# Optimization experiments

Measured on AMD Instinct MI355X. Metric: run time of the kernel, lower is better.

## Reference

```python
import jax, jax.numpy as jnp
import numpy as np

B, N, E, T, DS, H = 32, 1024, 16384, 8, 8, 32
EPS = 1e-12

def setup_inputs() -> dict:
    key = jax.random.key(0)
    ks = jax.random.split(key, 10)
    xyz = jax.random.normal(ks[0], (B, N, 3), dtype=jnp.float32)
    edge_index = jax.random.randint(ks[1], (2, E), 0, N)
    edge_type = jax.random.randint(ks[2], (E,), 0, T)
    edge_rest_lengths = jax.random.uniform(ks[3], (E,), dtype=jnp.float32) + 0.5
    type_emb = 0.1 * jax.random.normal(ks[4], (T, DS), dtype=jnp.float32)
    w1 = 0.1 * jax.random.normal(ks[5], (3 + DS, H), dtype=jnp.float32)
    b1 = jnp.zeros((H,), dtype=jnp.float32)
    w2 = 0.1 * jax.random.normal(ks[6], (H,), dtype=jnp.float32)
    b2 = jnp.zeros((1,), dtype=jnp.float32)
    default_bias = 0.1 * jax.random.normal(ks[7], (1,), dtype=jnp.float32)
    return {"xyz": xyz, "edge_index": edge_index, "edge_type": edge_type,
            "edge_rest_lengths": edge_rest_lengths, "type_emb": type_emb,
            "w1": w1, "b1": b1, "w2": w2, "b2": b2, "default_bias": default_bias}

def reference(xyz, edge_index, edge_type, edge_rest_lengths, type_emb, w1, b1, w2, b2, default_bias):
    src, dst = edge_index[0], edge_index[1]           # (E,)
    diff = xyz[:, dst, :] - xyz[:, src, :]            # (B,E,3) edge gather
    dist = jnp.sqrt(jnp.sum(diff * diff, axis=-1) + EPS)  # (B,E)
    rest = jnp.broadcast_to(edge_rest_lengths, dist.shape)  # (B,E)
    geo = jnp.stack([dist, rest, dist - rest], axis=-1)     # (B,E,3)
    struct = jnp.broadcast_to(type_emb[edge_type], (dist.shape[0], E, type_emb.shape[1]))  # (B,E,DS)
    feats = jnp.concatenate([geo, struct], axis=-1)   # (B,E,3+DS)
    h = jax.nn.relu(jnp.einsum('bef,fh->beh', feats, w1) + b1)  # (B,E,H)
    score = jnp.einsum('beh,h->be', h, w2) + b2       # (B,E)
    # dense bias with learnable default fill, symmetric edge scatter
    bias = default_bias * jnp.ones((xyz.shape[0], N, N), dtype=xyz.dtype)
    bias = bias.at[:, src, dst].set(score)
    bias = bias.at[:, dst, src].set(score)
    return bias[:, None, :, :]                        # (B,1,N,N)
```

## Files before the change

kernel.cpp:

```cpp
#include <hip/hip_runtime.h>

#define BB 32
#define NN 1024
#define EE 16384
#define DSS 8
#define HH 32


__global__ void init_prio(int* __restrict__ prio) {
    int idx = blockIdx.x * blockDim.x + threadIdx.x;
    ((int4*)prio)[idx] = make_int4(-1, -1, -1, -1);
}

__global__ void build_prio(const int* __restrict__ edge_index, int* __restrict__ prio) {
    int t = blockIdx.x * blockDim.x + threadIdx.x;
    int pass = t >= EE;
    int e = t - pass * EE;
    int src = edge_index[e];
    int dst = edge_index[EE + e];
    int i = pass ? dst : src;
    int j = pass ? src : dst;
    atomicMax(&prio[i * NN + j], t);
}

__global__ void score_kernel(const float* __restrict__ xyz,
                             const int* __restrict__ edge_index,
                             const int* __restrict__ edge_type,
                             const float* __restrict__ rest_len,
                             const float* __restrict__ type_emb,
                             const float* __restrict__ w1,
                             const float* __restrict__ b1,
                             const float* __restrict__ w2,
                             const float* __restrict__ b2,
                             float* __restrict__ score) {
    int idx = blockIdx.x * blockDim.x + threadIdx.x;
    int e = idx & (EE - 1);
    int b = idx >> 14;
    int src = edge_index[e];
    int dst = edge_index[EE + e];
    const float* ps = xyz + ((size_t)b * NN + src) * 3;
    const float* pd = xyz + ((size_t)b * NN + dst) * 3;
    float dx = pd[0] - ps[0];
    float dy = pd[1] - ps[1];
    float dz = pd[2] - ps[2];
    float dist = sqrtf(dx * dx + dy * dy + dz * dz + 1e-12f);
    float rest = rest_len[e];
    int ty = edge_type[e];
    float f0 = dist, f1 = rest, f2 = dist - rest;

    float emb[DSS];
#pragma unroll
    for (int k = 0; k < DSS; ++k) emb[k] = type_emb[ty * DSS + k];

    float acc = b2[0];
#pragma unroll
    for (int j = 0; j < HH; ++j) {
        float h = b1[j];
        h = fmaf(f0, w1[0 * HH + j], h);
        h = fmaf(f1, w1[1 * HH + j], h);
        h = fmaf(f2, w1[2 * HH + j], h);
#pragma unroll
        for (int k = 0; k < DSS; ++k)
            h = fmaf(emb[k], w1[(3 + k) * HH + j], h);
        h = fmaxf(h, 0.0f);
        acc = fmaf(w2[j], h, acc);
    }
    score[idx] = acc;
}

__global__ void fill_kernel(const int* __restrict__ prio,
                            const float* __restrict__ score,
                            const float* __restrict__ default_bias,
                            float* __restrict__ out) {
    int i = blockIdx.x;
    int j0 = threadIdx.x * 4;
    float defv = default_bias[0];
    int4 p = *(const int4*)(prio + (size_t)i * NN + j0);
    float* po = out + (size_t)i * NN + j0;

    if ((p.x & p.y & p.z & p.w) < 0) {
        float4 v = make_float4(defv, defv, defv, defv);
#pragma unroll 4
        for (int b = 0; b < BB; ++b)
            *(float4*)(po + (size_t)b * NN * NN) = v;
    } else {
        int ex = p.x & (EE - 1);
        int ey = p.y & (EE - 1);
        int ez = p.z & (EE - 1);
        int ew = p.w & (EE - 1);
        for (int b = 0; b < BB; ++b) {
            const float* sb = score + (size_t)b * EE;
            float4 v;
            v.x = (p.x >= 0) ? sb[ex] : defv;
            v.y = (p.y >= 0) ? sb[ey] : defv;
            v.z = (p.z >= 0) ? sb[ez] : defv;
            v.w = (p.w >= 0) ? sb[ew] : defv;
            *(float4*)(po + (size_t)b * NN * NN) = v;
        }
    }
}

extern "C" void kernel_launch(void* const* d_in, const int* in_sizes, int n_in,
                              void* d_out, int out_size, void* d_ws, size_t ws_size,
                              hipStream_t stream) {
    const float* xyz       = (const float*)d_in[0];
    const int*   edge_idx  = (const int*)  d_in[1];
    const int*   edge_type = (const int*)  d_in[2];
    const float* rest_len  = (const float*)d_in[3];
    const float* type_emb  = (const float*)d_in[4];
    const float* w1        = (const float*)d_in[5];
    const float* b1        = (const float*)d_in[6];
    const float* w2        = (const float*)d_in[7];
    const float* b2        = (const float*)d_in[8];
    const float* def_bias  = (const float*)d_in[9];
    float* out = (float*)d_out;

    int*   prio  = (int*)d_ws;
    float* score = (float*)((char*)d_ws + (size_t)NN * NN * 4);

    init_prio <<<(NN * NN / 4) / 256, 256, 0, stream>>>(prio);
    build_prio<<<(2 * EE) / 256,      256, 0, stream>>>(edge_idx, prio);
    score_kernel<<<(BB * EE) / 256,   256, 0, stream>>>(xyz, edge_idx, edge_type, rest_len,
                                                        type_emb, w1, b1, w2, b2, score);
    fill_kernel<<<NN, 256, 0, stream>>>(prio, score, def_bias, out);
}
```

Before: 213.8 us.

## Fuse prio init into score kernel and compact edge scatter in fill

Merges the priority-table initialization into the score kernel as extra blocks, cutting one launch. The fill kernel now splits the batch across two grid rows, writes the default value to every slot with unconditional float4 stores, and then uses a shared-memory list of the row's edge columns to scatter scores with scalar stores. This removes divergent per-element selects and gathers in the dense fill, at the cost of writing edge locations twice and relying on __syncthreads ordering for the overwrite.

Measured after the change: 179.0 us. 16.3% less time.

```diff
diff --git a/kernel.cpp b/kernel.cpp
--- a/kernel.cpp
+++ b/kernel.cpp
@@ -7,33 +7,25 @@
 #define HH 32
 
 
-__global__ void init_prio(int* __restrict__ prio) {
-    int idx = blockIdx.x * blockDim.x + threadIdx.x;
-    ((int4*)prio)[idx] = make_int4(-1, -1, -1, -1);
-}
-
-__global__ void build_prio(const int* __restrict__ edge_index, int* __restrict__ prio) {
-    int t = blockIdx.x * blockDim.x + threadIdx.x;
-    int pass = t >= EE;
-    int e = t - pass * EE;
-    int src = edge_index[e];
-    int dst = edge_index[EE + e];
-    int i = pass ? dst : src;
-    int j = pass ? src : dst;
-    atomicMax(&prio[i * NN + j], t);
-}
-
-__global__ void score_kernel(const float* __restrict__ xyz,
-                             const int* __restrict__ edge_index,
-                             const int* __restrict__ edge_type,
-                             const float* __restrict__ rest_len,
-                             const float* __restrict__ type_emb,
-                             const float* __restrict__ w1,
-                             const float* __restrict__ b1,
-                             const float* __restrict__ w2,
-                             const float* __restrict__ b2,
-                             float* __restrict__ score) {
-    int idx = blockIdx.x * blockDim.x + threadIdx.x;
+__global__ void prep_kernel(const float* __restrict__ xyz,
+                            const int* __restrict__ edge_index,
+                            const int* __restrict__ edge_type,
+                            const float* __restrict__ rest_len,
+                            const float* __restrict__ type_emb,
+                            const float* __restrict__ w1,
+                            const float* __restrict__ b1,
+                            const float* __restrict__ w2,
+                            const float* __restrict__ b2,
+                            float* __restrict__ score,
+                            int* __restrict__ prio) {
+    int blk = blockIdx.x;
+    int tid = threadIdx.x;
+    if (blk >= 2048) {
+        int idx = (blk - 2048) * 256 + tid;
+        ((int4*)prio)[idx] = make_int4(-1, -1, -1, -1);
+        return;
+    }
+    int idx = blk * 256 + tid;
     int e = idx & (EE - 1);
     int b = idx >> 14;
     int src = edge_index[e];
@@ -68,35 +60,51 @@
     score[idx] = acc;
 }
 
+__global__ void build_prio(const int* __restrict__ edge_index, int* __restrict__ prio) {
+    int t = blockIdx.x * blockDim.x + threadIdx.x;
+    int pass = t >= EE;
+    int e = t - pass * EE;
+    int src = edge_index[e];
+    int dst = edge_index[EE + e];
+    int i = pass ? dst : src;
+    int j = pass ? src : dst;
+    atomicMax(&prio[i * NN + j], t);
+}
+
 __global__ void fill_kernel(const int* __restrict__ prio,
                             const float* __restrict__ score,
                             const float* __restrict__ default_bias,
                             float* __restrict__ out) {
+    __shared__ int s_col[1024];
+    __shared__ int s_e[1024];
+    __shared__ int s_cnt;
     int i = blockIdx.x;
-    int j0 = threadIdx.x * 4;
+    int bg = blockIdx.y;
+    int tid = threadIdx.x;
+
+    if (tid == 0) s_cnt = 0;
+    __syncthreads();
+
+    int4 p = *(const int4*)(prio + (size_t)i * NN + tid * 4);
+    if (p.x >= 0) { int s = atomicAdd(&s_cnt, 1); s_col[s] = tid * 4 + 0; s_e[s] = p.x & (EE - 1); }
+    if (p.y >= 0) { int s = atomicAdd(&s_cnt, 1); s_col[s] = tid * 4 + 1; s_e[s] = p.y & (EE - 1); }
+    if (p.z >= 0) { int s = atomicAdd(&s_cnt, 1); s_col[s] = tid * 4 + 2; s_e[s] = p.z & (EE - 1); }
+    if (p.w >= 0) { int s = atomicAdd(&s_cnt, 1); s_col[s] = tid * 4 + 3; s_e[s] = p.w & (EE - 1); }
+
     float defv = default_bias[0];
-    int4 p = *(const int4*)(prio + (size_t)i * NN + j0);
-    float* po = out + (size_t)i * NN + j0;
+    float4 dv = make_float4(defv, defv, defv, defv);
+    float* base = out + (size_t)(bg * 16) * NN * NN + (size_t)i * NN + tid * 4;
+#pragma unroll
+    for (int bb = 0; bb < 16; ++bb)
+        *(float4*)(base + (size_t)bb * NN * NN) = dv;
 
-    if ((p.x & p.y & p.z & p.w) < 0) {
-        float4 v = make_float4(defv, defv, defv, defv);
-#pragma unroll 4
-        for (int b = 0; b < BB; ++b)
-            *(float4*)(po + (size_t)b * NN * NN) = v;
-    } else {
-        int ex = p.x & (EE - 1);
-        int ey = p.y & (EE - 1);
-        int ez = p.z & (EE - 1);
-        int ew = p.w & (EE - 1);
-        for (int b = 0; b < BB; ++b) {
-            const float* sb = score + (size_t)b * EE;
-            float4 v;
-            v.x = (p.x >= 0) ? sb[ex] : defv;
-            v.y = (p.y >= 0) ? sb[ey] : defv;
-            v.z = (p.z >= 0) ? sb[ez] : defv;
-            v.w = (p.w >= 0) ? sb[ew] : defv;
-            *(float4*)(po + (size_t)b * NN * NN) = v;
-        }
+    __syncthreads();
+
+    int total = s_cnt << 4;
+    for (int w = tid; w < total; w += 256) {
+        int c = w >> 4;
+        int b = (bg << 4) + (w & 15);
+        out[(size_t)b * NN * NN + (size_t)i * NN + s_col[c]] = score[(size_t)b * EE + s_e[c]];
     }
 }
 
@@ -118,9 +126,8 @@
     int*   prio  = (int*)d_ws;
     float* score = (float*)((char*)d_ws + (size_t)NN * NN * 4);
 
-    init_prio <<<(NN * NN / 4) / 256, 256, 0, stream>>>(prio);
-    build_prio<<<(2 * EE) / 256,      256, 0, stream>>>(edge_idx, prio);
-    score_kernel<<<(BB * EE) / 256,   256, 0, stream>>>(xyz, edge_idx, edge_type, rest_len,
-                                                        type_emb, w1, b1, w2, b2, score);
-    fill_kernel<<<NN, 256, 0, stream>>>(prio, score, def_bias, out);
+    prep_kernel<<<3072, 256, 0, stream>>>(xyz, edge_idx, edge_type, rest_len,
+                                          type_emb, w1, b1, w2, b2, score, prio);
+    build_prio<<<(2 * EE) / 256, 256, 0, stream>>>(edge_idx, prio);
+    fill_kernel<<<dim3(NN, 2), 256, 0, stream>>>(prio, score, def_bias, out);
 }
```
